# Performance work log

Hardware: AMD Instinct MI355X
Metric: run time of the kernel (lower is better)

## Reference

```python
import jax, jax.numpy as jnp
import numpy as np

LATENT_DIM = 128
KQ_DIM = 32
B, N, K = 8, 16384, 16


def setup_inputs() -> dict:
    key = jax.random.key(0)
    k1, k2, k3, k4, k5, k6 = jax.random.split(key, 6)
    features = jax.random.normal(k1, (B, N, LATENT_DIM), dtype=jnp.float32)
    ks_w = jax.random.normal(k2, (KQ_DIM, LATENT_DIM), dtype=jnp.float32) * (LATENT_DIM ** -0.5)
    ks_b = jax.random.normal(k3, (KQ_DIM,), dtype=jnp.float32) * 0.01
    qs_w = jax.random.normal(k4, (KQ_DIM, LATENT_DIM), dtype=jnp.float32) * (LATENT_DIM ** -0.5)
    qs_b = jax.random.normal(k5, (KQ_DIM,), dtype=jnp.float32) * 0.01
    indices = jax.random.randint(k6, (3, B, N, K), 0, N, dtype=jnp.int64)
    return {"features": features, "ks_w": ks_w, "ks_b": ks_b,
            "qs_w": qs_w, "qs_b": qs_b, "indices": indices}


def reference(features, ks_w, ks_b, qs_w, qs_b, indices):
    # features: [B, N, latent_dim]; indices: [3, B, N, K]
    b, n, _ = features.shape
    k = indices.shape[-1]
    # Linear projections (torch Linear: x @ W^T + b)
    flatten_ks = jnp.einsum('bnl,dl->bnd', features, ks_w) + ks_b  # [B,N,D]
    flatten_qs = jnp.einsum('bnl,dl->bnd', features, qs_w) + qs_b  # [B,N,D]
    d = flatten_ks.shape[-1]
    # gather along node dim N using index channels 1 (x) and 2 (y)
    x_idx = indices[1].reshape(b, n * k)  # [B, N*K]
    y_idx = indices[2].reshape(b, n * k)
    x_features = jnp.take_along_axis(flatten_ks, x_idx[..., None], axis=1).reshape(b, n, k, d)
    y_features = jnp.take_along_axis(flatten_qs, y_idx[..., None], axis=1).reshape(b, n, k, d)
    # scaled dot-product affinity
    logits = jnp.sum(x_features * y_features, axis=-1) * (d ** -0.5)  # [B,N,K]
    return logits
```

## Files before the change

### kernel.cpp

```cpp
#include <hip/hip_runtime.h>

#define BATCH   8
#define NNODES  16384
#define KNBR    16
#define LATENT  128
#define DOUT    32
#define NROWS   (BATCH * NNODES)

typedef __attribute__((ext_vector_type(8))) short short8;
typedef __attribute__((ext_vector_type(4))) float floatx4;

__device__ __forceinline__ unsigned short f2bf(float f) {
    unsigned u = __float_as_uint(f);
    u += 0x7fff + ((u >> 16) & 1);
    return (unsigned short)(u >> 16);
}

__device__ __forceinline__ float dot2bf(unsigned a, unsigned b) {
    float alo = __uint_as_float(a << 16);
    float ahi = __uint_as_float(a & 0xffff0000u);
    float blo = __uint_as_float(b << 16);
    float bhi = __uint_as_float(b & 0xffff0000u);
    return alo * blo + ahi * bhi;
}

__device__ __forceinline__ void gload_lds16(const float* g, void* l) {
    __builtin_amdgcn_global_load_lds(
        (const __attribute__((address_space(1))) void*)g,
        (__attribute__((address_space(3))) void*)l,
        16, 0, 0);
}

#define BPAD 136

__global__ __launch_bounds__(256) void proj_kernel(
    const float* __restrict__ feats,
    const float* __restrict__ kw, const float* __restrict__ kb,
    const float* __restrict__ qw, const float* __restrict__ qb,
    unsigned short* __restrict__ tkb, unsigned short* __restrict__ tqb)
{
    __shared__ __align__(16) unsigned char A_raw[128 * 256];
    __shared__ unsigned short B_lds[64 * BPAD];
    __shared__ float bias_lds[64];

    const int tid  = threadIdx.x;
    const int lane = tid & 63;
    const int w    = tid >> 6;
    const int bat  = blockIdx.x & 7;
    const int u    = blockIdx.x >> 3;
    const long long blk_row = (long long)bat * NNODES + (long long)u * 128;

    {
        const float4* kw4 = (const float4*)kw;
        const float4* qw4 = (const float4*)qw;
#pragma unroll
        for (int i = 0; i < 8; ++i) {
            const int linear = i * 256 + tid;
            const int row = linear >> 5;
            const int c4  = linear & 31;
            const float4 v = (row < 32) ? kw4[row * 32 + c4] : qw4[(row - 32) * 32 + c4];
            unsigned lo = f2bf(v.x) | ((unsigned)f2bf(v.y) << 16);
            unsigned hi = f2bf(v.z) | ((unsigned)f2bf(v.w) << 16);
            *(uint2*)&B_lds[row * BPAD + c4 * 4] = make_uint2(lo, hi);
        }
        if (tid < 64) bias_lds[tid] = (tid < 32) ? kb[tid] : qb[tid - 32];
    }

    const int m = lane & 15;
    const int q = lane >> 4;

    floatx4 acc[2][4];
#pragma unroll
    for (int rt = 0; rt < 2; ++rt)
#pragma unroll
        for (int ct = 0; ct < 4; ++ct) acc[rt][ct] = (floatx4){0.f, 0.f, 0.f, 0.f};

    for (int ch = 0; ch < 2; ++ch) {
        if (ch) __syncthreads();

#pragma unroll
        for (int i = 0; i < 8; ++i) {
            const int L  = i * 4096 + tid * 16;
            const int r  = L >> 8;
            const int c0 = (((L & 255) ^ ((r & 7) << 4)) >> 2);
            gload_lds16(feats + (blk_row + r) * 128 + ch * 64 + c0, A_raw + L);
        }
        __syncthreads();

#pragma unroll
        for (int ks = 0; ks < 2; ++ks) {
            const int kg = ch * 64 + ks * 32 + q * 8;
            short8 bf[4];
#pragma unroll
            for (int ct = 0; ct < 4; ++ct)
                bf[ct] = *(const short8*)&B_lds[(ct * 16 + m) * BPAD + kg];
#pragma unroll
            for (int rt = 0; rt < 2; ++rt) {
                const int rloc = w * 32 + rt * 16 + m;
                const int b0   = rloc * 256 + ks * 128 + q * 32;
                const int p0   = b0 ^ ((rloc & 7) << 4);
                const float4 a0 = *(const float4*)(A_raw + p0);
                const float4 a1 = *(const float4*)(A_raw + (p0 ^ 16));
                union { short8 s; unsigned uu[4]; } af;
                af.uu[0] = f2bf(a0.x) | ((unsigned)f2bf(a0.y) << 16);
                af.uu[1] = f2bf(a0.z) | ((unsigned)f2bf(a0.w) << 16);
                af.uu[2] = f2bf(a1.x) | ((unsigned)f2bf(a1.y) << 16);
                af.uu[3] = f2bf(a1.z) | ((unsigned)f2bf(a1.w) << 16);
#pragma unroll
                for (int ct = 0; ct < 4; ++ct)
                    acc[rt][ct] = __builtin_amdgcn_mfma_f32_16x16x32_bf16(af.s, bf[ct], acc[rt][ct], 0, 0, 0);
            }
        }
    }

#pragma unroll
    for (int rt = 0; rt < 2; ++rt) {
#pragma unroll
        for (int reg = 0; reg < 4; ++reg) {
            const long long row = blk_row + w * 32 + rt * 16 + q * 4 + reg;
#pragma unroll
            for (int ct = 0; ct < 4; ++ct) {
                const float val = acc[rt][ct][reg] + bias_lds[ct * 16 + m];
                if (ct < 2) tkb[row * DOUT + ct * 16 + m]       = f2bf(val);
                else        tqb[row * DOUT + (ct - 2) * 16 + m] = f2bf(val);
            }
        }
    }
}

__global__ __launch_bounds__(256) void gather_dot_kernel(
    const unsigned short* __restrict__ tkb, const unsigned short* __restrict__ tqb,
    const int* __restrict__ idx, float* __restrict__ out)
{
    const long long NK  = (long long)NNODES * KNBR;
    const long long BNK = NK * BATCH;

    const int bat  = blockIdx.x & 7;
    const int blk  = blockIdx.x >> 3;
    const int tid  = threadIdx.x;
    const int lane = tid & 63;
    const int j    = tid & 3;

    const uint4* tb_k = (const uint4*)(tkb + (long long)bat * NNODES * DOUT);
    const uint4* tb_q = (const uint4*)(tqb + (long long)bat * NNODES * DOUT);

    const long long o0 = (long long)bat * NK + (long long)blk * 256 + tid;

    const int xi = __builtin_nontemporal_load(&idx[BNK + o0]);
    const int yi = __builtin_nontemporal_load(&idx[2 * BNK + o0]);

    float r0, r1, r2, r3;
#pragma unroll
    for (int p = 0; p < 4; ++p) {
        const int xp = __shfl(xi, (lane & ~3) | p);
        const int yp = __shfl(yi, (lane & ~3) | p);
        const uint4 x = tb_k[(long long)xp * 4 + j];
        const uint4 y = tb_q[(long long)yp * 4 + j];
        float s = dot2bf(x.x, y.x) + dot2bf(x.y, y.y)
                + dot2bf(x.z, y.z) + dot2bf(x.w, y.w);
        s += __shfl_xor(s, 1);
        s += __shfl_xor(s, 2);
        if      (p == 0) r0 = s;
        else if (p == 1) r1 = s;
        else if (p == 2) r2 = s;
        else             r3 = s;
    }
    const float v = (j == 0) ? r0 : (j == 1) ? r1 : (j == 2) ? r2 : r3;
    __builtin_nontemporal_store(v * 0.17677669529663687f, &out[o0]);
}

extern "C" void kernel_launch(void* const* d_in, const int* in_sizes, int n_in,
                              void* d_out, int out_size, void* d_ws, size_t ws_size,
                              hipStream_t stream)
{
    const float* feats = (const float*)d_in[0];
    const float* kw    = (const float*)d_in[1];
    const float* kb    = (const float*)d_in[2];
    const float* qw    = (const float*)d_in[3];
    const float* qb    = (const float*)d_in[4];
    const int*   idx   = (const int*)d_in[5];
    float*       out   = (float*)d_out;

    unsigned short* tkb = (unsigned short*)d_ws;
    unsigned short* tqb = tkb + (long long)NROWS * DOUT;

    proj_kernel<<<NROWS / 128, 256, 0, stream>>>(feats, kw, kb, qw, qb, tkb, tqb);
    gather_dot_kernel<<<(int)((long long)BATCH * NNODES * KNBR / 256), 256, 0, stream>>>(
        tkb, tqb, idx, out);
}
```

Before: 144.0 us.

## Load projection A-operand directly from global into registers, dropping LDS staging

The projection kernel no longer stages feature tiles in LDS with the global_load_lds path and XOR swizzle. Each lane now loads its own MFMA A-fragment straight from global memory into registers, issuing all loads up front before the weight-tile barrier, and converts them to bf16 once. This removes 32 KB of LDS per block and one barrier, which should allow more blocks per CU and overlap the feature loads with the weight setup. The cost is higher register pressure and per-lane 32-byte strided global accesses instead of fully coalesced block loads.

```diff
diff --git a/kernel.cpp b/kernel.cpp
--- a/kernel.cpp
+++ b/kernel.cpp
@@ -16,19 +16,16 @@
     return (unsigned short)(u >> 16);
 }
 
+__device__ __forceinline__ unsigned pack2bf(float a, float b) {
+    return (unsigned)f2bf(a) | ((unsigned)f2bf(b) << 16);
+}
+
 __device__ __forceinline__ float dot2bf(unsigned a, unsigned b) {
     float alo = __uint_as_float(a << 16);
     float ahi = __uint_as_float(a & 0xffff0000u);
     float blo = __uint_as_float(b << 16);
     float bhi = __uint_as_float(b & 0xffff0000u);
     return alo * blo + ahi * bhi;
-}
-
-__device__ __forceinline__ void gload_lds16(const float* g, void* l) {
-    __builtin_amdgcn_global_load_lds(
-        (const __attribute__((address_space(1))) void*)g,
-        (__attribute__((address_space(3))) void*)l,
-        16, 0, 0);
 }
 
 #define BPAD 136
@@ -39,7 +36,6 @@
     const float* __restrict__ qw, const float* __restrict__ qb,
     unsigned short* __restrict__ tkb, unsigned short* __restrict__ tqb)
 {
-    __shared__ __align__(16) unsigned char A_raw[128 * 256];
     __shared__ unsigned short B_lds[64 * BPAD];
     __shared__ float bias_lds[64];
 
@@ -59,9 +55,8 @@
             const int row = linear >> 5;
             const int c4  = linear & 31;
             const float4 v = (row < 32) ? kw4[row * 32 + c4] : qw4[(row - 32) * 32 + c4];
-            unsigned lo = f2bf(v.x) | ((unsigned)f2bf(v.y) << 16);
-            unsigned hi = f2bf(v.z) | ((unsigned)f2bf(v.w) << 16);
-            *(uint2*)&B_lds[row * BPAD + c4 * 4] = make_uint2(lo, hi);
+            *(uint2*)&B_lds[row * BPAD + c4 * 4] =
+                make_uint2(pack2bf(v.x, v.y), pack2bf(v.z, v.w));
         }
         if (tid < 64) bias_lds[tid] = (tid < 32) ? kb[tid] : qb[tid - 32];
     }
@@ -69,48 +64,51 @@
     const int m = lane & 15;
     const int q = lane >> 4;
 
+    const float4* Ar0 = (const float4*)(feats + (blk_row + w * 32 + m) * 128);
+    const float4* Ar1 = (const float4*)(feats + (blk_row + w * 32 + 16 + m) * 128);
+    float4 araw[2][4][2];
+#pragma unroll
+    for (int ks = 0; ks < 4; ++ks) {
+        const int f4o = ks * 8 + q * 2;
+        araw[0][ks][0] = Ar0[f4o];
+        araw[0][ks][1] = Ar0[f4o + 1];
+        araw[1][ks][0] = Ar1[f4o];
+        araw[1][ks][1] = Ar1[f4o + 1];
+    }
+
+    short8 afr[2][4];
+#pragma unroll
+    for (int rt = 0; rt < 2; ++rt)
+#pragma unroll
+        for (int ks = 0; ks < 4; ++ks) {
+            union { short8 s; unsigned uu[4]; } af;
+            af.uu[0] = pack2bf(araw[rt][ks][0].x, araw[rt][ks][0].y);
+            af.uu[1] = pack2bf(araw[rt][ks][0].z, araw[rt][ks][0].w);
+            af.uu[2] = pack2bf(araw[rt][ks][1].x, araw[rt][ks][1].y);
+            af.uu[3] = pack2bf(araw[rt][ks][1].z, araw[rt][ks][1].w);
+            afr[rt][ks] = af.s;
+        }
+
+    __syncthreads();
+
     floatx4 acc[2][4];
 #pragma unroll
     for (int rt = 0; rt < 2; ++rt)
 #pragma unroll
         for (int ct = 0; ct < 4; ++ct) acc[rt][ct] = (floatx4){0.f, 0.f, 0.f, 0.f};
 
-    for (int ch = 0; ch < 2; ++ch) {
-        if (ch) __syncthreads();
-
 #pragma unroll
-        for (int i = 0; i < 8; ++i) {
-            const int L  = i * 4096 + tid * 16;
-            const int r  = L >> 8;
-            const int c0 = (((L & 255) ^ ((r & 7) << 4)) >> 2);
-            gload_lds16(feats + (blk_row + r) * 128 + ch * 64 + c0, A_raw + L);
-        }
-        __syncthreads();
-
+    for (int ks = 0; ks < 4; ++ks) {
+        const int kg = ks * 32 + q * 8;
+        short8 bf[4];
 #pragma unroll
-        for (int ks = 0; ks < 2; ++ks) {
-            const int kg = ch * 64 + ks * 32 + q * 8;
-            short8 bf[4];
+        for (int ct = 0; ct < 4; ++ct)
+            bf[ct] = *(const short8*)&B_lds[(ct * 16 + m) * BPAD + kg];
+#pragma unroll
+        for (int rt = 0; rt < 2; ++rt)
 #pragma unroll
             for (int ct = 0; ct < 4; ++ct)
-                bf[ct] = *(const short8*)&B_lds[(ct * 16 + m) * BPAD + kg];
-#pragma unroll
-            for (int rt = 0; rt < 2; ++rt) {
-                const int rloc = w * 32 + rt * 16 + m;
-                const int b0   = rloc * 256 + ks * 128 + q * 32;
-                const int p0   = b0 ^ ((rloc & 7) << 4);
-                const float4 a0 = *(const float4*)(A_raw + p0);
-                const float4 a1 = *(const float4*)(A_raw + (p0 ^ 16));
-                union { short8 s; unsigned uu[4]; } af;
-                af.uu[0] = f2bf(a0.x) | ((unsigned)f2bf(a0.y) << 16);
-                af.uu[1] = f2bf(a0.z) | ((unsigned)f2bf(a0.w) << 16);
-                af.uu[2] = f2bf(a1.x) | ((unsigned)f2bf(a1.y) << 16);
-                af.uu[3] = f2bf(a1.z) | ((unsigned)f2bf(a1.w) << 16);
-#pragma unroll
-                for (int ct = 0; ct < 4; ++ct)
-                    acc[rt][ct] = __builtin_amdgcn_mfma_f32_16x16x32_bf16(af.s, bf[ct], acc[rt][ct], 0, 0, 0);
-            }
-        }
+                acc[rt][ct] = __builtin_amdgcn_mfma_f32_16x16x32_bf16(afr[rt][ks], bf[ct], acc[rt][ct], 0, 0, 0);
     }
 
 #pragma unroll
```

Measured after the change: 145.9 us. No clear change (+1.4%).
